# Kernel tuning notes

Hardware: AMD Instinct MI355X
Metric: run time of the kernel (lower is better)

## Reference

```python
import jax, jax.numpy as jnp
import numpy as np

B, L, C, H = 2, 2048, 1024, 16
D = C // H
THETA = 50000.0


def rotate_half(x):
    x1, x2 = jnp.split(x, 2, axis=-1)
    return jnp.concatenate((-x2, x1), axis=-1)


def rope_freqs(n, dim):
    inv_freq = 1.0 / (THETA ** (jnp.arange(0, dim, 2, dtype=jnp.float32) / dim))
    freqs = jnp.arange(n, dtype=jnp.float32)[:, None] * inv_freq[None, :]  # [n, dim//2]
    return jnp.concatenate((freqs, freqs), axis=-1)  # [n, dim]


def setup_inputs() -> dict:
    key = jax.random.key(0)
    ks = jax.random.split(key, 8)
    q = jax.random.normal(ks[0], (B, L, C), dtype=jnp.float32)
    mask = jax.random.randint(ks[1], (B, L), 0, 2) > 0
    mask = mask.at[:, 0].set(True)  # avoid fully-masked rows
    s = 1.0 / np.sqrt(C)
    Wq = jax.random.normal(ks[2], (C, C), dtype=jnp.float32) * s
    Wk = jax.random.normal(ks[3], (C, C), dtype=jnp.float32) * s
    Wv = jax.random.normal(ks[4], (C, C), dtype=jnp.float32) * s
    Wo = jax.random.normal(ks[5], (C, C), dtype=jnp.float32) * s
    bo = jnp.zeros((C,), dtype=jnp.float32)
    return {"q": q, "mask": mask, "Wq": Wq, "Wk": Wk, "Wv": Wv, "Wo": Wo, "bo": bo}


def reference(q, mask, Wq, Wk, Wv, Wo, bo):
    x = q
    # QKV projections (torch Linear: y = x @ W.T)
    def proj(W):
        y = jnp.einsum('blc,oc->blo', x, W)
        return y.reshape(B, L, H, D).transpose(0, 2, 1, 3)  # [B,H,L,D]
    qh, kh, vh = proj(Wq), proj(Wk), proj(Wv)
    # RoPE (L == S)
    pos = rope_freqs(L, D)  # [L, D]
    cos, sin = jnp.cos(pos), jnp.sin(pos)
    qh = qh * cos + rotate_half(qh) * sin
    kh = kh * cos + rotate_half(kh) * sin
    # masked SDPA with additive bias (-inf where mask is False)
    scale = 1.0 / np.sqrt(D)
    bias = jnp.where(mask[:, None, None, :], 0.0, -jnp.inf)  # [B,1,1,S]
    scores = jnp.einsum('bhld,bhsd->bhls', qh, kh) * scale + bias
    attn = jax.nn.softmax(scores, axis=-1)
    out = jnp.einsum('bhls,bhsd->bhld', attn, vh)
    out = out.transpose(0, 2, 1, 3).reshape(B, L, C)
    return jnp.einsum('blc,oc->blo', out, Wo) + bo
```

## Files before the change

kernel.cpp:

```cpp
#include <hip/hip_runtime.h>
#include <hip/hip_bf16.h>

typedef __hip_bfloat16 bf16;
typedef short bf16x8 __attribute__((ext_vector_type(8)));
typedef short bf16x4 __attribute__((ext_vector_type(4)));
typedef float floatx4 __attribute__((ext_vector_type(4)));

#define Bb 2
#define Ll 2048
#define Cc 1024
#define Hh 16
#define Dd 64
#define INVFREQ_LN 0.3381180763f
#define QSCALE 0.125f
#define NCONV 4096

#define GLD16(gp, lp) __builtin_amdgcn_global_load_lds( \
    (const __attribute__((address_space(1))) void*)(gp), \
    (__attribute__((address_space(3))) void*)(lp), 16, 0, 0)

__device__ inline short f2bf(float f) {
    __hip_bfloat16 h = __float2bfloat16(f);
    return *reinterpret_cast<short*>(&h);
}
__device__ inline short f2bf_rn(float f) {
    return (short)((__float_as_uint(f) + 0x8000u) >> 16);
}

__global__ __launch_bounds__(256) void convert_scan(
    const float* __restrict__ x, const float* __restrict__ wq,
    const float* __restrict__ wk, const float* __restrict__ wv,
    const float* __restrict__ wo,
    bf16* __restrict__ xb, bf16* __restrict__ wqkv, bf16* __restrict__ wob,
    const int* __restrict__ mask, int* __restrict__ cidx, int* __restrict__ valid)
{
    if (blockIdx.x >= NCONV) {
        const int b   = blockIdx.x - NCONV;
        const int tid = threadIdx.x;
        const int base = b * Ll + tid * 8;
        int m[8]; int s = 0;
        #pragma unroll
        for (int i = 0; i < 8; i++) { m[i] = mask[base + i] ? 1 : 0; s += m[i]; }
        const int lane = tid & 63;
        int xx = s;
        #pragma unroll
        for (int off = 1; off < 64; off <<= 1) {
            int y = __shfl_up(xx, off);
            if (lane >= off) xx += y;
        }
        __shared__ int wtot[4];
        if (lane == 63) wtot[tid >> 6] = xx;
        __syncthreads();
        int wbase = 0;
        const int w = tid >> 6;
        #pragma unroll
        for (int i = 0; i < 4; i++) if (i < w) wbase += wtot[i];
        int run = wbase + (xx - s);
        #pragma unroll
        for (int i = 0; i < 8; i++) { cidx[base + i] = run; run += m[i]; }
        if (tid == 255) valid[b] = run;
        return;
    }

    const int XN = (Bb * Ll * Cc) / 8;
    const int WN = (Cc * Cc) / 8;
    int i = blockIdx.x * 256 + threadIdx.x;
    const float* src; bf16* dst;
    if (i < XN)               { src = x  + (size_t)i * 8;                 dst = xb   + (size_t)i * 8; }
    else if (i < XN + WN)     { int j = i - XN;        src = wq + (size_t)j * 8; dst = wqkv + (size_t)j * 8; }
    else if (i < XN + 2*WN)   { int j = i - XN - WN;   src = wk + (size_t)j * 8; dst = wqkv + (size_t)Cc*Cc     + (size_t)j * 8; }
    else if (i < XN + 3*WN)   { int j = i - XN - 2*WN; src = wv + (size_t)j * 8; dst = wqkv + (size_t)Cc*Cc*2   + (size_t)j * 8; }
    else                      { int j = i - XN - 3*WN; src = wo + (size_t)j * 8; dst = wob  + (size_t)j * 8; }
    float4 a = *reinterpret_cast<const float4*>(src);
    float4 b = *reinterpret_cast<const float4*>(src + 4);
    float vv[8] = {a.x, a.y, a.z, a.w, b.x, b.y, b.z, b.w};
    bf16x8 o;
    #pragma unroll
    for (int t = 0; t < 8; t++) o[t] = f2bf(vv[t]);
    *reinterpret_cast<bf16x8*>(dst) = o;
}

template <int ROWS, int NTHREADS>
__device__ __forceinline__ void stage_swz(const bf16* __restrict__ g, int ldk,
                                          short* lds, int tid)
{
    #pragma unroll
    for (int s = 0; s < (ROWS * 4) / NTHREADS; s++) {
        const int idx = s * NTHREADS + tid;
        const int r   = idx >> 2;
        const int col = ((idx & 3) ^ ((r >> 1) & 3)) << 3;
        GLD16(g + (size_t)r * ldk + col, lds + idx * 8);
    }
}

#define VMCNT(N) asm volatile("s_waitcnt vmcnt(" #N ")" ::: "memory")

__global__ __launch_bounds__(512, 4) void gemm_qkv(
    const bf16* __restrict__ A, const bf16* __restrict__ W,
    bf16* __restrict__ qb, bf16* __restrict__ kb, bf16* __restrict__ vb,
    const int* __restrict__ cmask, const int* __restrict__ cidx)
{
    constexpr int K = Cc;
    constexpr int T = K / 32;

    __shared__ __align__(16) short As[3][128 * 32];
    __shared__ __align__(16) short Bs[3][256 * 32];

    const int tid  = threadIdx.x;
    const int wave = tid >> 6;
    const int lane = tid & 63;
    const int l15  = lane & 15;
    const int quad = lane >> 4;
    const int wm   = wave & 1;
    const int wn   = wave >> 1;

    const int lin = blockIdx.y * 12 + blockIdx.x;
    const int swz = (lin & 7) * 48 + (lin >> 3);
    const int m0  = (swz / 12) * 128;
    const int n0  = (swz % 12) * 256;

    const bf16* Ag = A + (size_t)m0 * K;
    const bf16* Wg = W + (size_t)n0 * K;

    const int gsw = (quad ^ ((l15 >> 1) & 3)) << 3;

    floatx4 acc[4][4];
    #pragma unroll
    for (int mt = 0; mt < 4; mt++)
        #pragma unroll
        for (int nt = 0; nt < 4; nt++)
            #pragma unroll
            for (int r = 0; r < 4; r++) acc[mt][nt][r] = 0.f;

    stage_swz<128, 512>(Ag,      K, &As[0][0], tid);
    stage_swz<256, 512>(Wg,      K, &Bs[0][0], tid);
    stage_swz<128, 512>(Ag + 32, K, &As[1][0], tid);
    stage_swz<256, 512>(Wg + 32, K, &Bs[1][0], tid);
    VMCNT(3);
    __builtin_amdgcn_s_barrier();

    int cur = 0;
    for (int t = 0; t < T; t++) {
        const short* Ac = &As[0][0] + cur * (128 * 32);
        const short* Bc = &Bs[0][0] + cur * (256 * 32);

        if (t + 2 < T) {
            int nb = cur + 2; if (nb >= 3) nb -= 3;
            const int kk = (t + 2) << 5;
            stage_swz<128, 512>(Ag + kk, K, &As[nb][0], tid);
            stage_swz<256, 512>(Wg + kk, K, &Bs[nb][0], tid);
        }

        bf16x8 af[4], bfr[4];
        #pragma unroll
        for (int mt = 0; mt < 4; mt++)
            af[mt] = *(const bf16x8*)(Ac + (wm * 64 + mt * 16 + l15) * 32 + gsw);
        #pragma unroll
        for (int nt = 0; nt < 4; nt++)
            bfr[nt] = *(const bf16x8*)(Bc + (wn * 64 + nt * 16 + l15) * 32 + gsw);

        __builtin_amdgcn_s_setprio(1);
        #pragma unroll
        for (int mt = 0; mt < 4; mt++)
            #pragma unroll
            for (int nt = 0; nt < 4; nt++)
                acc[mt][nt] = __builtin_amdgcn_mfma_f32_16x16x32_bf16(
                    af[mt], bfr[nt], acc[mt][nt], 0, 0, 0);
        __builtin_amdgcn_s_setprio(0);

        if (t + 2 < T) { VMCNT(3); }
        else           { VMCNT(0); }
        __builtin_amdgcn_s_barrier();

        cur++; if (cur == 3) cur = 0;
    }

    const int colbase = n0 + wn * 64;
    const int which   = colbase >> 10;
    const int hh      = (colbase & (Cc - 1)) >> 6;
    if (which == 2) {
        #pragma unroll
        for (int mt = 0; mt < 4; mt++)
            #pragma unroll
            for (int r = 0; r < 4; r++) {
                int row = m0 + wm * 64 + mt * 16 + quad * 4 + r;
                int b = row >> 11, l = row & (Ll - 1);
                if (cmask[b * Ll + l]) {
                    int c = cidx[b * Ll + l];
                    size_t head = (size_t)(b * Hh + hh) * Dd * Ll;
                    int lbase = (c & ~63) | (c & 7);
                    int lg    = (c >> 3) & 7;
                    #pragma unroll
                    for (int nt = 0; nt < 4; nt++) {
                        int d = nt * 16 + l15;
                        int pos = lbase | ((lg ^ (d & 7)) << 3);
                        vb[head + (size_t)d * Ll + pos] = __float2bfloat16(acc[mt][nt][r]);
                    }
                }
            }
    } else {
        bf16* dst = which ? kb : qb;
        const float qs = which ? 1.0f : QSCALE;
        const float base0 = __expf(-(float)l15 * INVFREQ_LN);
        const float base1 = __expf(-(float)(l15 + 16) * INVFREQ_LN);
        #pragma unroll
        for (int mt = 0; mt < 4; mt++)
            #pragma unroll
            for (int r = 0; r < 4; r++) {
                int row = m0 + wm * 64 + mt * 16 + quad * 4 + r;
                int b = row >> 11, l = row & (Ll - 1);
                int cm = 1, c = l;
                if (which == 1) {
                    cm = cmask[b * Ll + l];
                    c  = cidx[b * Ll + l];
                }
                if (cm) {
                    size_t rb = ((size_t)(b * Hh + hh) * Ll + c) * Dd;
                    #pragma unroll
                    for (int nt2 = 0; nt2 < 2; nt2++) {
                        float fr = (float)l * (nt2 ? base1 : base0);
                        float sn, cs;
                        __sincosf(fr, &sn, &cs);
                        float x1 = acc[mt][nt2][r];
                        float x2 = acc[mt][nt2 + 2][r];
                        float o1 = (x1 * cs - x2 * sn) * qs;
                        float o2 = (x2 * cs + x1 * sn) * qs;
                        int d1 = nt2 * 16 + l15;
                        int d2 = d1 + 32;
                        if (which == 1) {
                            int sw = c & 7;
                            int a1 = ((((d1 >> 3) ^ sw)) << 3) | (d1 & 7);
                            int a2 = ((((d2 >> 3) ^ sw)) << 3) | (d2 & 7);
                            dst[rb + a1] = __float2bfloat16(o1);
                            dst[rb + a2] = __float2bfloat16(o2);
                        } else {
                            dst[rb + d1] = __float2bfloat16(o1);
                            dst[rb + d2] = __float2bfloat16(o2);
                        }
                    }
                }
            }
    }
}

__global__ __launch_bounds__(256, 4) void gemm_out(
    const bf16* __restrict__ A, const bf16* __restrict__ W,
    float* __restrict__ outf, const float* __restrict__ bias)
{
    constexpr int K = Cc, N = Cc;
    constexpr int T = K / 32;

    __shared__ __align__(16) short As[3][64 * 32];
    __shared__ __align__(16) short Bs[3][64 * 32];

    const int tid  = threadIdx.x;
    const int wave = tid >> 6;
    const int lane = tid & 63;
    const int l15  = lane & 15;
    const int quad = lane >> 4;
    const int wm   = wave >> 1;
    const int wn   = wave & 1;

    const int lin = blockIdx.y * 16 + blockIdx.x;
    const int swz = (lin & 7) * 128 + (lin >> 3);
    const int m0  = (swz >> 4) * 64;
    const int n0  = (swz & 15) * 64;

    const bf16* Ag = A + (size_t)m0 * K;
    const bf16* Wg = W + (size_t)n0 * K;

    const int gsw = (quad ^ ((l15 >> 1) & 3)) << 3;

    floatx4 acc[2][2];
    #pragma unroll
    for (int mt = 0; mt < 2; mt++)
        #pragma unroll
        for (int nt = 0; nt < 2; nt++)
            #pragma unroll
            for (int r = 0; r < 4; r++) acc[mt][nt][r] = 0.f;

    stage_swz<64, 256>(Ag,      K, &As[0][0], tid);
    stage_swz<64, 256>(Wg,      K, &Bs[0][0], tid);
    stage_swz<64, 256>(Ag + 32, K, &As[1][0], tid);
    stage_swz<64, 256>(Wg + 32, K, &Bs[1][0], tid);
    VMCNT(2);
    __builtin_amdgcn_s_barrier();

    int cur = 0;
    for (int t = 0; t < T; t++) {
        const short* Ac = &As[0][0] + cur * (64 * 32);
        const short* Bc = &Bs[0][0] + cur * (64 * 32);

        if (t + 2 < T) {
            int nb = cur + 2; if (nb >= 3) nb -= 3;
            const int kk = (t + 2) << 5;
            stage_swz<64, 256>(Ag + kk, K, &As[nb][0], tid);
            stage_swz<64, 256>(Wg + kk, K, &Bs[nb][0], tid);
        }

        bf16x8 af[2], bfr[2];
        #pragma unroll
        for (int mt = 0; mt < 2; mt++)
            af[mt] = *(const bf16x8*)(Ac + (wm * 32 + mt * 16 + l15) * 32 + gsw);
        #pragma unroll
        for (int nt = 0; nt < 2; nt++)
            bfr[nt] = *(const bf16x8*)(Bc + (wn * 32 + nt * 16 + l15) * 32 + gsw);

        __builtin_amdgcn_s_setprio(1);
        #pragma unroll
        for (int mt = 0; mt < 2; mt++)
            #pragma unroll
            for (int nt = 0; nt < 2; nt++)
                acc[mt][nt] = __builtin_amdgcn_mfma_f32_16x16x32_bf16(
                    af[mt], bfr[nt], acc[mt][nt], 0, 0, 0);
        __builtin_amdgcn_s_setprio(0);

        if (t + 2 < T) { VMCNT(2); }
        else           { VMCNT(0); }
        __builtin_amdgcn_s_barrier();

        cur++; if (cur == 3) cur = 0;
    }

    #pragma unroll
    for (int mt = 0; mt < 2; mt++)
        #pragma unroll
        for (int r = 0; r < 4; r++) {
            int row = m0 + wm * 32 + mt * 16 + quad * 4 + r;
            #pragma unroll
            for (int nt = 0; nt < 2; nt++) {
                int col = n0 + wn * 32 + nt * 16 + l15;
                outf[(size_t)row * N + col] = acc[mt][nt][r] + bias[col];
            }
        }
}

#define LSTR 72

__global__ __launch_bounds__(512) void attn_mfma(
    const bf16* __restrict__ q, const bf16* __restrict__ k, const bf16* __restrict__ vt,
    const int* __restrict__ valid, bf16* __restrict__ ctx)
{
    __shared__ __align__(16) short Ks[2][64 * 64];
    __shared__ __align__(16) short Vs[2][64 * 64];
    __shared__ __align__(16) short Ps[8][16 * LSTR];

    const int tid  = threadIdx.x;
    const int wave = tid >> 6;
    const int lane = tid & 63;
    const int l15  = lane & 15;
    const int quad = lane >> 4;

    const int bh = blockIdx.x & 31;
    const int q0 = (blockIdx.x >> 5) << 7;
    const int b  = bh >> 4;
    const int h  = bh & (Hh - 1);

    const int nvalid = valid[b];
    const int ntiles = (nvalid + 63) >> 6;

    const short* qb  = (const short*)(q  + (size_t)bh * Ll * Dd);
    const short* kb  = (const short*)(k  + (size_t)bh * Ll * Dd);
    const short* vtb = (const short*)(vt + (size_t)bh * Dd * Ll);

    const int qrow = q0 + wave * 16 + l15;
    bf16x8 qa0 = *(const bf16x8*)(qb + (size_t)qrow * Dd + quad * 8);
    bf16x8 qa1 = *(const bf16x8*)(qb + (size_t)qrow * Dd + 32 + quad * 8);

    const int g0 = ((quad ^ (l15 & 7)) << 3);
    const int g1 = (((quad + 4) ^ (l15 & 7)) << 3);

    const short* vgp = vtb + (size_t)(tid >> 3) * Ll + ((tid & 7) << 3);
    short* ksl = &Ks[0][0] + tid * 8;
    short* vsl = &Vs[0][0] + tid * 8;
    const int lbuf = 64 * 64;

    floatx4 O[4];
    float l_r = 0.f;
    #pragma unroll
    for (int nt = 0; nt < 4; nt++)
        #pragma unroll
        for (int r = 0; r < 4; r++) O[nt][r] = 0.f;

    GLD16(kb + tid * 8, ksl);
    GLD16(vgp, vsl);

    for (int t = 0; t < ntiles; t++) {
        const int cur = t & 1;
        __syncthreads();
        if (t + 1 < ntiles) {
            const int s1 = (t + 1) << 6;
            GLD16(kb + (size_t)s1 * Dd + tid * 8, ksl + (cur ^ 1) * lbuf);
            GLD16(vgp + s1,                       vsl + (cur ^ 1) * lbuf);
        }

        const short* Kc = &Ks[cur][0];
        const short* Vc = &Vs[cur][0];
        floatx4 S[4];
        #pragma unroll
        for (int nt = 0; nt < 4; nt++) {
            const short* krow = Kc + (nt * 16 + l15) * 64;
            bf16x8 ka0 = *(const bf16x8*)(krow + g0);
            bf16x8 ka1 = *(const bf16x8*)(krow + g1);
            floatx4 acc; acc[0] = acc[1] = acc[2] = acc[3] = 0.f;
            acc = __builtin_amdgcn_mfma_f32_16x16x32_bf16(ka0, qa0, acc, 0, 0, 0);
            acc = __builtin_amdgcn_mfma_f32_16x16x32_bf16(ka1, qa1, acc, 0, 0, 0);
            S[nt] = acc;
        }

        if (t + 1 < ntiles) {
            #pragma unroll
            for (int nt = 0; nt < 4; nt++) {
                bf16x4 pw;
                #pragma unroll
                for (int r = 0; r < 4; r++) {
                    float p = __expf(S[nt][r]);
                    l_r += p;
                    pw[r] = f2bf_rn(p);
                }
                *(bf16x4*)&Ps[wave][l15 * LSTR + nt * 16 + quad * 4] = pw;
            }
        } else {
            const int kbase = (t << 6) + quad * 4;
            #pragma unroll
            for (int nt = 0; nt < 4; nt++) {
                bf16x4 pw;
                #pragma unroll
                for (int r = 0; r < 4; r++) {
                    float p = (kbase + nt * 16 + r < nvalid) ? __expf(S[nt][r]) : 0.f;
                    l_r += p;
                    pw[r] = f2bf_rn(p);
                }
                *(bf16x4*)&Ps[wave][l15 * LSTR + nt * 16 + quad * 4] = pw;
            }
        }

        bf16x8 pb0 = *(const bf16x8*)&Ps[wave][l15 * LSTR + quad * 8];
        bf16x8 pb1 = *(const bf16x8*)&Ps[wave][l15 * LSTR + 32 + quad * 8];
        #pragma unroll
        for (int nt = 0; nt < 4; nt++) {
            const short* vrow = Vc + (nt * 16 + l15) * 64;
            bf16x8 va0 = *(const bf16x8*)(vrow + g0);
            bf16x8 va1 = *(const bf16x8*)(vrow + g1);
            O[nt] = __builtin_amdgcn_mfma_f32_16x16x32_bf16(va0, pb0, O[nt], 0, 0, 0);
            O[nt] = __builtin_amdgcn_mfma_f32_16x16x32_bf16(va1, pb1, O[nt], 0, 0, 0);
        }
    }

    float l = l_r;
    l += __shfl_xor(l, 16);
    l += __shfl_xor(l, 32);
    const float inv = 1.0f / l;

    {
        int row = q0 + wave * 16 + l15;
        short* cp = (short*)ctx + ((size_t)(b * Ll + row)) * Cc + h * Dd;
        #pragma unroll
        for (int nt = 0; nt < 4; nt++) {
            bf16x4 ov;
            #pragma unroll
            for (int r = 0; r < 4; r++) ov[r] = f2bf_rn(O[nt][r] * inv);
            *(bf16x4*)&cp[nt * 16 + quad * 4] = ov;
        }
    }
}

extern "C" void kernel_launch(void* const* d_in, const int* in_sizes, int n_in,
                              void* d_out, int out_size, void* d_ws, size_t ws_size,
                              hipStream_t stream) {
    const float* x    = (const float*)d_in[0];
    const int*   mask = (const int*)d_in[1];
    const float* Wq   = (const float*)d_in[2];
    const float* Wk   = (const float*)d_in[3];
    const float* Wv   = (const float*)d_in[4];
    const float* Wo   = (const float*)d_in[5];
    const float* bo   = (const float*)d_in[6];
    float* out = (float*)d_out;

    const size_t per = (size_t)Bb * Hh * Ll * Dd;
    bf16* qbuf = (bf16*)d_ws;
    bf16* kbuf = qbuf + per;
    bf16* vbuf = kbuf + per;
    bf16* xb   = vbuf + per;
    bf16* wqkv = xb + per;
    bf16* wob  = wqkv + (size_t)3 * Cc * Cc;
    int*  cidx   = (int*)(wob + (size_t)Cc * Cc);
    int*  cvalid = cidx + Bb * Ll;
    bf16* ctx  = xb;

    const int M = Bb * Ll;

    convert_scan<<<NCONV + Bb, 256, 0, stream>>>(
        x, Wq, Wk, Wv, Wo, xb, wqkv, wob, mask, cidx, cvalid);

    dim3 gQKV(3 * Cc / 256, M / 128);
    gemm_qkv<<<gQKV, 512, 0, stream>>>(xb, wqkv, qbuf, kbuf, vbuf, mask, cidx);

    attn_mfma<<<Bb * Hh * (Ll / 128), 512, 0, stream>>>(qbuf, kbuf, vbuf, cvalid, ctx);

    dim3 gOut(Cc / 64, M / 64);
    gemm_out<<<gOut, 256, 0, stream>>>(ctx, wob, out, bo);
}
```

Measured before the change: 176.2 us.

## Shrink QKV GEMM tile to 128x128 and widen attention KV tile to 128

The QKV GEMM moves from 512-thread 128x256 tiles to 256-thread 128x128 tiles with a 24-column grid swizzle. This doubles the block count and lowers per-block LDS, which is meant to improve occupancy and tail balance. The attention kernel now loads 128 keys per pipeline stage, using explicit vmcnt waits and a raw barrier instead of __syncthreads. It also replaces the padded P staging buffer with an XOR-swizzled layout, aiming to halve barrier and sync overhead per key and avoid LDS bank conflicts. The trade-offs are doubled LDS use in attention and more masked-tail work when the valid length is not a multiple of 128.

```diff
diff --git a/kernel.cpp b/kernel.cpp
--- a/kernel.cpp
+++ b/kernel.cpp
@@ -95,7 +95,7 @@
 
 #define VMCNT(N) asm volatile("s_waitcnt vmcnt(" #N ")" ::: "memory")
 
-__global__ __launch_bounds__(512, 4) void gemm_qkv(
+__global__ __launch_bounds__(256, 3) void gemm_qkv(
     const bf16* __restrict__ A, const bf16* __restrict__ W,
     bf16* __restrict__ qb, bf16* __restrict__ kb, bf16* __restrict__ vb,
     const int* __restrict__ cmask, const int* __restrict__ cidx)
@@ -104,20 +104,20 @@
     constexpr int T = K / 32;
 
     __shared__ __align__(16) short As[3][128 * 32];
-    __shared__ __align__(16) short Bs[3][256 * 32];
+    __shared__ __align__(16) short Bs[3][128 * 32];
 
     const int tid  = threadIdx.x;
     const int wave = tid >> 6;
     const int lane = tid & 63;
     const int l15  = lane & 15;
     const int quad = lane >> 4;
-    const int wm   = wave & 1;
-    const int wn   = wave >> 1;
-
-    const int lin = blockIdx.y * 12 + blockIdx.x;
-    const int swz = (lin & 7) * 48 + (lin >> 3);
-    const int m0  = (swz / 12) * 128;
-    const int n0  = (swz % 12) * 256;
+    const int wm   = wave >> 1;
+    const int wn   = wave & 1;
+
+    const int lin = blockIdx.y * 24 + blockIdx.x;
+    const int swz = (lin & 7) * 96 + (lin >> 3);
+    const int m0  = (swz / 24) * 128;
+    const int n0  = (swz % 24) * 128;
 
     const bf16* Ag = A + (size_t)m0 * K;
     const bf16* Wg = W + (size_t)n0 * K;
@@ -132,32 +132,32 @@
             #pragma unroll
             for (int r = 0; r < 4; r++) acc[mt][nt][r] = 0.f;
 
-    stage_swz<128, 512>(Ag,      K, &As[0][0], tid);
-    stage_swz<256, 512>(Wg,      K, &Bs[0][0], tid);
-    stage_swz<128, 512>(Ag + 32, K, &As[1][0], tid);
-    stage_swz<256, 512>(Wg + 32, K, &Bs[1][0], tid);
-    VMCNT(3);
+    stage_swz<128, 256>(Ag,      K, &As[0][0], tid);
+    stage_swz<128, 256>(Wg,      K, &Bs[0][0], tid);
+    stage_swz<128, 256>(Ag + 32, K, &As[1][0], tid);
+    stage_swz<128, 256>(Wg + 32, K, &Bs[1][0], tid);
+    VMCNT(4);
     __builtin_amdgcn_s_barrier();
 
     int cur = 0;
     for (int t = 0; t < T; t++) {
         const short* Ac = &As[0][0] + cur * (128 * 32);
-        const short* Bc = &Bs[0][0] + cur * (256 * 32);
+        const short* Bc = &Bs[0][0] + cur * (128 * 32);
 
         if (t + 2 < T) {
             int nb = cur + 2; if (nb >= 3) nb -= 3;
             const int kk = (t + 2) << 5;
-            stage_swz<128, 512>(Ag + kk, K, &As[nb][0], tid);
-            stage_swz<256, 512>(Wg + kk, K, &Bs[nb][0], tid);
+            stage_swz<128, 256>(Ag + kk, K, &As[nb][0], tid);
+            stage_swz<128, 256>(Wg + kk, K, &Bs[nb][0], tid);
         }
 
         bf16x8 af[4], bfr[4];
+        #pragma unroll
+        for (int nt = 0; nt < 4; nt++)
+            bfr[nt] = *(const bf16x8*)(Bc + (wn * 64 + nt * 16 + l15) * 32 + gsw);
         #pragma unroll
         for (int mt = 0; mt < 4; mt++)
             af[mt] = *(const bf16x8*)(Ac + (wm * 64 + mt * 16 + l15) * 32 + gsw);
-        #pragma unroll
-        for (int nt = 0; nt < 4; nt++)
-            bfr[nt] = *(const bf16x8*)(Bc + (wn * 64 + nt * 16 + l15) * 32 + gsw);
 
         __builtin_amdgcn_s_setprio(1);
         #pragma unroll
@@ -168,7 +168,7 @@
                     af[mt], bfr[nt], acc[mt][nt], 0, 0, 0);
         __builtin_amdgcn_s_setprio(0);
 
-        if (t + 2 < T) { VMCNT(3); }
+        if (t + 2 < T) { VMCNT(4); }
         else           { VMCNT(0); }
         __builtin_amdgcn_s_barrier();
 
@@ -335,15 +335,15 @@
         }
 }
 
-#define LSTR 72
+#define KVB 128
 
 __global__ __launch_bounds__(512) void attn_mfma(
     const bf16* __restrict__ q, const bf16* __restrict__ k, const bf16* __restrict__ vt,
     const int* __restrict__ valid, bf16* __restrict__ ctx)
 {
-    __shared__ __align__(16) short Ks[2][64 * 64];
-    __shared__ __align__(16) short Vs[2][64 * 64];
-    __shared__ __align__(16) short Ps[8][16 * LSTR];
+    __shared__ __align__(16) short Ks[2][KVB * 64];
+    __shared__ __align__(16) short Vs[2][KVB * 64];
+    __shared__ __align__(16) short Ps[8][16 * 64];
 
     const int tid  = threadIdx.x;
     const int wave = tid >> 6;
@@ -357,7 +357,7 @@
     const int h  = bh & (Hh - 1);
 
     const int nvalid = valid[b];
-    const int ntiles = (nvalid + 63) >> 6;
+    const int ntiles = (nvalid + KVB - 1) >> 7;
 
     const short* qb  = (const short*)(q  + (size_t)bh * Ll * Dd);
     const short* kb  = (const short*)(k  + (size_t)bh * Ll * Dd);
@@ -373,7 +373,7 @@
     const short* vgp = vtb + (size_t)(tid >> 3) * Ll + ((tid & 7) << 3);
     short* ksl = &Ks[0][0] + tid * 8;
     short* vsl = &Vs[0][0] + tid * 8;
-    const int lbuf = 64 * 64;
+    const int lbuf = KVB * 64;
 
     floatx4 O[4];
     float l_r = 0.f;
@@ -382,68 +382,84 @@
         #pragma unroll
         for (int r = 0; r < 4; r++) O[nt][r] = 0.f;
 
-    GLD16(kb + tid * 8, ksl);
-    GLD16(vgp, vsl);
+    GLD16(kb + tid * 8,        ksl);
+    GLD16(kb + 4096 + tid * 8, ksl + 4096);
+    GLD16(vgp,                 vsl);
+    GLD16(vgp + 64,            vsl + 4096);
+
+    short* Pw = &Ps[wave][0];
 
     for (int t = 0; t < ntiles; t++) {
         const int cur = t & 1;
-        __syncthreads();
+        __builtin_amdgcn_s_barrier();
         if (t + 1 < ntiles) {
-            const int s1 = (t + 1) << 6;
-            GLD16(kb + (size_t)s1 * Dd + tid * 8, ksl + (cur ^ 1) * lbuf);
-            GLD16(vgp + s1,                       vsl + (cur ^ 1) * lbuf);
+            const size_t s1 = (size_t)(t + 1) * KVB;
+            GLD16(kb + s1 * 64 + tid * 8,        ksl + (cur ^ 1) * lbuf);
+            GLD16(kb + s1 * 64 + 4096 + tid * 8, ksl + (cur ^ 1) * lbuf + 4096);
+            GLD16(vgp + s1,                      vsl + (cur ^ 1) * lbuf);
+            GLD16(vgp + s1 + 64,                 vsl + (cur ^ 1) * lbuf + 4096);
+            VMCNT(4);
+        } else {
+            VMCNT(0);
         }
 
         const short* Kc = &Ks[cur][0];
         const short* Vc = &Vs[cur][0];
-        floatx4 S[4];
-        #pragma unroll
-        for (int nt = 0; nt < 4; nt++) {
-            const short* krow = Kc + (nt * 16 + l15) * 64;
-            bf16x8 ka0 = *(const bf16x8*)(krow + g0);
-            bf16x8 ka1 = *(const bf16x8*)(krow + g1);
-            floatx4 acc; acc[0] = acc[1] = acc[2] = acc[3] = 0.f;
-            acc = __builtin_amdgcn_mfma_f32_16x16x32_bf16(ka0, qa0, acc, 0, 0, 0);
-            acc = __builtin_amdgcn_mfma_f32_16x16x32_bf16(ka1, qa1, acc, 0, 0, 0);
-            S[nt] = acc;
-        }
-
-        if (t + 1 < ntiles) {
+
+        #pragma unroll
+        for (int c = 0; c < 2; c++) {
+            floatx4 S[4];
             #pragma unroll
             for (int nt = 0; nt < 4; nt++) {
-                bf16x4 pw;
+                const short* krow = Kc + (c * 64 + nt * 16 + l15) * 64;
+                bf16x8 ka0 = *(const bf16x8*)(krow + g0);
+                bf16x8 ka1 = *(const bf16x8*)(krow + g1);
+                floatx4 acc; acc[0] = acc[1] = acc[2] = acc[3] = 0.f;
+                acc = __builtin_amdgcn_mfma_f32_16x16x32_bf16(ka0, qa0, acc, 0, 0, 0);
+                acc = __builtin_amdgcn_mfma_f32_16x16x32_bf16(ka1, qa1, acc, 0, 0, 0);
+                S[nt] = acc;
+            }
+
+            const int kglob0 = t * KVB + c * 64;
+            if (kglob0 + 64 <= nvalid) {
                 #pragma unroll
-                for (int r = 0; r < 4; r++) {
-                    float p = __expf(S[nt][r]);
-                    l_r += p;
-                    pw[r] = f2bf_rn(p);
+                for (int nt = 0; nt < 4; nt++) {
+                    bf16x4 pw;
+                    #pragma unroll
+                    for (int r = 0; r < 4; r++) {
+                        float p = __expf(S[nt][r]);
+                        l_r += p;
+                        pw[r] = f2bf_rn(p);
+                    }
+                    int grp = (2 * nt + (quad >> 1)) ^ (l15 & 7);
+                    *(bf16x4*)&Pw[l15 * 64 + (grp << 3) + ((quad & 1) << 2)] = pw;
                 }
-                *(bf16x4*)&Ps[wave][l15 * LSTR + nt * 16 + quad * 4] = pw;
+            } else {
+                const int kb0 = kglob0 + quad * 4;
+                #pragma unroll
+                for (int nt = 0; nt < 4; nt++) {
+                    bf16x4 pw;
+                    #pragma unroll
+                    for (int r = 0; r < 4; r++) {
+                        float p = (kb0 + nt * 16 + r < nvalid) ? __expf(S[nt][r]) : 0.f;
+                        l_r += p;
+                        pw[r] = f2bf_rn(p);
+                    }
+                    int grp = (2 * nt + (quad >> 1)) ^ (l15 & 7);
+                    *(bf16x4*)&Pw[l15 * 64 + (grp << 3) + ((quad & 1) << 2)] = pw;
+                }
             }
-        } else {
-            const int kbase = (t << 6) + quad * 4;
+
+            bf16x8 pb0 = *(const bf16x8*)&Pw[l15 * 64 + ((quad ^ (l15 & 7)) << 3)];
+            bf16x8 pb1 = *(const bf16x8*)&Pw[l15 * 64 + (((4 + quad) ^ (l15 & 7)) << 3)];
             #pragma unroll
             for (int nt = 0; nt < 4; nt++) {
-                bf16x4 pw;
-                #pragma unroll
-                for (int r = 0; r < 4; r++) {
-                    float p = (kbase + nt * 16 + r < nvalid) ? __expf(S[nt][r]) : 0.f;
-                    l_r += p;
-                    pw[r] = f2bf_rn(p);
-                }
-                *(bf16x4*)&Ps[wave][l15 * LSTR + nt * 16 + quad * 4] = pw;
+                const short* vrow = Vc + c * 4096 + (nt * 16 + l15) * 64;
+                bf16x8 va0 = *(const bf16x8*)(vrow + g0);
+                bf16x8 va1 = *(const bf16x8*)(vrow + g1);
+                O[nt] = __builtin_amdgcn_mfma_f32_16x16x32_bf16(va0, pb0, O[nt], 0, 0, 0);
+                O[nt] = __builtin_amdgcn_mfma_f32_16x16x32_bf16(va1, pb1, O[nt], 0, 0, 0);
             }
-        }
-
-        bf16x8 pb0 = *(const bf16x8*)&Ps[wave][l15 * LSTR + quad * 8];
-        bf16x8 pb1 = *(const bf16x8*)&Ps[wave][l15 * LSTR + 32 + quad * 8];
-        #pragma unroll
-        for (int nt = 0; nt < 4; nt++) {
-            const short* vrow = Vc + (nt * 16 + l15) * 64;
-            bf16x8 va0 = *(const bf16x8*)(vrow + g0);
-            bf16x8 va1 = *(const bf16x8*)(vrow + g1);
-            O[nt] = __builtin_amdgcn_mfma_f32_16x16x32_bf16(va0, pb0, O[nt], 0, 0, 0);
-            O[nt] = __builtin_amdgcn_mfma_f32_16x16x32_bf16(va1, pb1, O[nt], 0, 0, 0);
         }
     }
 
@@ -493,8 +509,8 @@
     convert_scan<<<NCONV + Bb, 256, 0, stream>>>(
         x, Wq, Wk, Wv, Wo, xb, wqkv, wob, mask, cidx, cvalid);
 
-    dim3 gQKV(3 * Cc / 256, M / 128);
-    gemm_qkv<<<gQKV, 512, 0, stream>>>(xb, wqkv, qbuf, kbuf, vbuf, mask, cidx);
+    dim3 gQKV(3 * Cc / 128, M / 128);
+    gemm_qkv<<<gQKV, 256, 0, stream>>>(xb, wqkv, qbuf, kbuf, vbuf, mask, cidx);
 
     attn_mfma<<<Bb * Hh * (Ll / 128), 512, 0, stream>>>(qbuf, kbuf, vbuf, cvalid, ctx);
 
```

Result: no change. 173.7 us (-1.4%).
